# Kernel optimization log

Measured on AMD Instinct MI355X. Metric: run time of the kernel, lower is better.

The kernel has to match this reference:

```python
import jax, jax.numpy as jnp
import numpy as np

B, L, R = 4, 2048, 1024        # batch, seq_len, residual_dim
HID, EXP, K = 64, 2, 3          # hidden_dim, expansion_factor, conv_kernel_size
D = HID * EXP                   # ssm_input_dim = 128
N = HID                         # SSM state size = 64


def setup_inputs() -> dict:
    key = jax.random.key(0)
    ks = jax.random.split(key, 16)
    g = lambda k, s: jax.random.normal(k, s, dtype=jnp.float32) * 0.02
    inp = {
        "up_x":   jax.random.normal(ks[0], (B, L, R), dtype=jnp.float32),
        "W_up":   g(ks[1], (R, 2 * D)),
        "b_up":   g(ks[2], (2 * D,)),
        "conv_w": g(ks[3], (D, K)),          # depthwise Conv1d weight [C,1,K] squeezed
        "conv_b": g(ks[4], (D,)),
        "W_delta": g(ks[5], (D, D)),
        "b_delta": g(ks[6], (D,)),
        "W_B":    g(ks[7], (D, N)),
        "b_B":    g(ks[8], (N,)),
        "W_C":    g(ks[9], (D, N)),
        "b_C":    g(ks[10], (N,)),
        "A_log":  jnp.log(jnp.broadcast_to(jnp.arange(1, N + 1, dtype=jnp.float32), (D, N))),
        "D_skip": jnp.ones((D,), dtype=jnp.float32),
        "W_down": g(ks[11], (D, R)),
        "b_down": g(ks[12], (R,)),
    }
    return inp


def reference(up_x, W_up, b_up, conv_w, conv_b, W_delta, b_delta,
              W_B, b_B, W_C, b_C, A_log, D_skip, W_down, b_down):
    Lq = up_x.shape[1]
    u = up_x @ W_up + b_up                               # [B,L,2D]
    left, right = jnp.split(u, 2, axis=-1)               # each [B,L,D]

    # causal depthwise conv (pad left K-1, truncate to L)
    xp = jnp.pad(left, ((0, 0), (K - 1, 0), (0, 0)))     # [B,L+K-1,D]
    conv = sum(conv_w[:, k] * xp[:, k:k + Lq, :] for k in range(K)) + conv_b
    x = jax.nn.silu(conv)                                # [B,L,D]

    # S6 selective scan
    delta = jax.nn.softplus(x @ W_delta + b_delta)       # [B,L,D]
    Bm = x @ W_B + b_B                                   # [B,L,N]
    Cm = x @ W_C + b_C                                   # [B,L,N]
    A = -jnp.exp(A_log)                                  # [D,N]
    dA = jnp.exp(delta[..., None] * A)                   # [B,L,D,N]
    dBx = delta[..., None] * Bm[:, :, None, :] * x[..., None]  # [B,L,D,N]

    def step(h, inputs):
        dA_t, dBx_t, C_t = inputs                        # [B,D,N],[B,D,N],[B,N]
        h = dA_t * h + dBx_t
        y_t = jnp.einsum('bdn,bn->bd', h, C_t)
        return h, y_t

    h0 = jnp.zeros((up_x.shape[0], D, N), dtype=x.dtype)
    _, ys = jax.lax.scan(step, h0, (jnp.swapaxes(dA, 0, 1),
                                    jnp.swapaxes(dBx, 0, 1),
                                    jnp.swapaxes(Cm, 0, 1)))
    y = jnp.swapaxes(ys, 0, 1) + D_skip * x              # [B,L,D]

    gated = y * jax.nn.silu(right)                       # SiLU gate
    return gated @ W_down + b_down                       # [B,L,R]
```

## Files before the change

### kernel.cpp

```cpp
#include <hip/hip_runtime.h>
#include <math.h>

#define B_ 4
#define L_ 2048
#define R_ 1024
#define D_ 128
#define N_ 64
#define TWO_D 256
#define M_ (B_*L_)

#define LSTR 68

typedef __attribute__((ext_vector_type(8))) short bf16x8;
typedef __attribute__((ext_vector_type(4))) float f32x4;

__device__ __forceinline__ float silu_f(float z) {
    return z / (1.0f + __expf(-z));
}

__device__ __forceinline__ float softplus_f(float z) {
    return fmaxf(z, 0.0f) + log1pf(__expf(-fabsf(z)));
}

__device__ __forceinline__ short f2bf(float f) {
    union { float f; unsigned int u; } v; v.f = f;
    unsigned int r = v.u + 0x7FFF + ((v.u >> 16) & 1);
    return (short)(r >> 16);
}

__global__ __launch_bounds__(256) void gemm_up_mfma(
    const float* __restrict__ A,
    const float* __restrict__ W,
    const float* __restrict__ bias,
    float* __restrict__ C)
{
    __shared__ short Al[64 * LSTR];
    __shared__ short Bl[64 * LSTR];

    int lid = blockIdx.x;
    int xcd = lid & 7;
    int slot = lid >> 3;
    int bm = xcd * 16 + (slot >> 2);
    int bn = slot & 3;

    int tid = threadIdx.x;
    int w = tid >> 6, l = tid & 63;
    int lm = l & 15, q = l >> 4;
    int wm = (w & 1) * 32, wn = (w >> 1) * 32;

    f32x4 acc00 = {0,0,0,0}, acc01 = {0,0,0,0}, acc10 = {0,0,0,0}, acc11 = {0,0,0,0};

    int ar = tid >> 2, ak = (tid & 3) * 8;
    int bcol = tid & 63, bk = (tid >> 6) * 8;

    const float* Ag = A + (size_t)(bm * 64 + ar) * 1024 + ak;
    const float* Wg = W + (size_t)bn * 64 + bcol;

    for (int kt = 0; kt < 1024; kt += 32) {
        float4 a0 = *(const float4*)(Ag + kt);
        float4 a1 = *(const float4*)(Ag + kt + 4);
        bf16x8 ap;
        ap[0] = f2bf(a0.x); ap[1] = f2bf(a0.y); ap[2] = f2bf(a0.z); ap[3] = f2bf(a0.w);
        ap[4] = f2bf(a1.x); ap[5] = f2bf(a1.y); ap[6] = f2bf(a1.z); ap[7] = f2bf(a1.w);
        *(bf16x8*)&Al[ar * LSTR + ak] = ap;

        bf16x8 bp;
        #pragma unroll
        for (int j = 0; j < 8; j++)
            bp[j] = f2bf(Wg[(size_t)(kt + bk + j) * TWO_D]);
        *(bf16x8*)&Bl[bcol * LSTR + bk] = bp;

        __syncthreads();

        bf16x8 af0 = *(bf16x8*)&Al[(wm + lm) * LSTR + q * 8];
        bf16x8 af1 = *(bf16x8*)&Al[(wm + 16 + lm) * LSTR + q * 8];
        bf16x8 bf0 = *(bf16x8*)&Bl[(wn + lm) * LSTR + q * 8];
        bf16x8 bf1 = *(bf16x8*)&Bl[(wn + 16 + lm) * LSTR + q * 8];

        acc00 = __builtin_amdgcn_mfma_f32_16x16x32_bf16(af0, bf0, acc00, 0, 0, 0);
        acc01 = __builtin_amdgcn_mfma_f32_16x16x32_bf16(af0, bf1, acc01, 0, 0, 0);
        acc10 = __builtin_amdgcn_mfma_f32_16x16x32_bf16(af1, bf0, acc10, 0, 0, 0);
        acc11 = __builtin_amdgcn_mfma_f32_16x16x32_bf16(af1, bf1, acc11, 0, 0, 0);

        __syncthreads();
    }

    #pragma unroll
    for (int i = 0; i < 4; i++) {
        int r0 = bm * 64 + wm + q * 4 + i;
        int r1 = r0 + 16;
        int c0 = bn * 64 + wn + lm;
        int c1 = c0 + 16;
        C[(size_t)r0 * TWO_D + c0] = acc00[i] + bias[c0];
        C[(size_t)r0 * TWO_D + c1] = acc01[i] + bias[c1];
        C[(size_t)r1 * TWO_D + c0] = acc10[i] + bias[c0];
        C[(size_t)r1 * TWO_D + c1] = acc11[i] + bias[c1];
    }
}

__global__ __launch_bounds__(256) void conv_silu_kernel(
    const float* __restrict__ u,
    const float* __restrict__ conv_w,
    const float* __restrict__ conv_b,
    float* __restrict__ x)
{
    int idx = blockIdx.x * 256 + threadIdx.x;
    if (idx >= M_ * D_) return;
    int r = idx >> 7;
    int c = idx & 127;
    int t = r & (L_ - 1);

    float w0 = conv_w[c * 3 + 0];
    float w1 = conv_w[c * 3 + 1];
    float w2 = conv_w[c * 3 + 2];

    float v2 = u[(size_t)r * TWO_D + c];
    float v1 = (t >= 1) ? u[(size_t)(r - 1) * TWO_D + c] : 0.0f;
    float v0 = (t >= 2) ? u[(size_t)(r - 2) * TWO_D + c] : 0.0f;

    float z = fmaf(w0, v0, fmaf(w1, v1, fmaf(w2, v2, conv_b[c])));
    x[idx] = silu_f(z);
}

__global__ __launch_bounds__(256) void proj_mfma(
    const float* __restrict__ x,
    const float* __restrict__ W_delta, const float* __restrict__ b_delta,
    const float* __restrict__ W_B,     const float* __restrict__ b_B,
    const float* __restrict__ W_C,     const float* __restrict__ b_C,
    float* __restrict__ delta,
    float* __restrict__ Bm,
    float* __restrict__ Cm)
{
    __shared__ short Al[64 * LSTR];
    __shared__ short Bl[64 * LSTR];

    int lid = blockIdx.x;
    int xcd = lid & 7;
    int slot = lid >> 3;
    int bm = xcd * 16 + (slot >> 2);
    int bn = slot & 3;

    const float* Wsel; const float* bsel; int wstride;
    if (bn < 2)       { Wsel = W_delta + bn * 64; bsel = b_delta + bn * 64; wstride = 128; }
    else if (bn == 2) { Wsel = W_B;               bsel = b_B;               wstride = 64;  }
    else              { Wsel = W_C;               bsel = b_C;               wstride = 64;  }

    int tid = threadIdx.x;
    int w = tid >> 6, l = tid & 63;
    int lm = l & 15, q = l >> 4;
    int wm = (w & 1) * 32, wn = (w >> 1) * 32;

    f32x4 acc00 = {0,0,0,0}, acc01 = {0,0,0,0}, acc10 = {0,0,0,0}, acc11 = {0,0,0,0};

    int ar = tid >> 2, ak = (tid & 3) * 8;
    int bcol = tid & 63, bk = (tid >> 6) * 8;

    const float* Ag = x + (size_t)(bm * 64 + ar) * D_ + ak;
    const float* Wg = Wsel + bcol;

    for (int kt = 0; kt < 128; kt += 32) {
        float4 a0 = *(const float4*)(Ag + kt);
        float4 a1 = *(const float4*)(Ag + kt + 4);
        bf16x8 ap;
        ap[0] = f2bf(a0.x); ap[1] = f2bf(a0.y); ap[2] = f2bf(a0.z); ap[3] = f2bf(a0.w);
        ap[4] = f2bf(a1.x); ap[5] = f2bf(a1.y); ap[6] = f2bf(a1.z); ap[7] = f2bf(a1.w);
        *(bf16x8*)&Al[ar * LSTR + ak] = ap;

        bf16x8 bp;
        #pragma unroll
        for (int j = 0; j < 8; j++)
            bp[j] = f2bf(Wg[(size_t)(kt + bk + j) * wstride]);
        *(bf16x8*)&Bl[bcol * LSTR + bk] = bp;

        __syncthreads();

        bf16x8 af0 = *(bf16x8*)&Al[(wm + lm) * LSTR + q * 8];
        bf16x8 af1 = *(bf16x8*)&Al[(wm + 16 + lm) * LSTR + q * 8];
        bf16x8 bf0 = *(bf16x8*)&Bl[(wn + lm) * LSTR + q * 8];
        bf16x8 bf1 = *(bf16x8*)&Bl[(wn + 16 + lm) * LSTR + q * 8];

        acc00 = __builtin_amdgcn_mfma_f32_16x16x32_bf16(af0, bf0, acc00, 0, 0, 0);
        acc01 = __builtin_amdgcn_mfma_f32_16x16x32_bf16(af0, bf1, acc01, 0, 0, 0);
        acc10 = __builtin_amdgcn_mfma_f32_16x16x32_bf16(af1, bf0, acc10, 0, 0, 0);
        acc11 = __builtin_amdgcn_mfma_f32_16x16x32_bf16(af1, bf1, acc11, 0, 0, 0);

        __syncthreads();
    }

    #pragma unroll
    for (int i = 0; i < 4; i++) {
        int r0 = bm * 64 + wm + q * 4 + i;
        int r1 = r0 + 16;
        int c0 = wn + lm;
        int c1 = c0 + 16;
        float v00 = acc00[i] + bsel[c0];
        float v01 = acc01[i] + bsel[c1];
        float v10 = acc10[i] + bsel[c0];
        float v11 = acc11[i] + bsel[c1];
        if (bn < 2) {
            int cc0 = bn * 64 + c0, cc1 = bn * 64 + c1;
            delta[(size_t)r0 * D_ + cc0] = softplus_f(v00);
            delta[(size_t)r0 * D_ + cc1] = softplus_f(v01);
            delta[(size_t)r1 * D_ + cc0] = softplus_f(v10);
            delta[(size_t)r1 * D_ + cc1] = softplus_f(v11);
        } else if (bn == 2) {
            Bm[(size_t)r0 * N_ + c0] = v00;
            Bm[(size_t)r0 * N_ + c1] = v01;
            Bm[(size_t)r1 * N_ + c0] = v10;
            Bm[(size_t)r1 * N_ + c1] = v11;
        } else {
            Cm[(size_t)r0 * N_ + c0] = v00;
            Cm[(size_t)r0 * N_ + c1] = v01;
            Cm[(size_t)r1 * N_ + c0] = v10;
            Cm[(size_t)r1 * N_ + c1] = v11;
        }
    }
}

template<int LOG_NC>
__global__ __launch_bounds__(256) void scan_sumA(
    const float* __restrict__ delta,
    const float* __restrict__ x,
    const float* __restrict__ Bm,
    const float* __restrict__ A_log,
    float* __restrict__ ch_aprod,
    float* __restrict__ ch_h)
{
    constexpr int NCt = 1 << LOG_NC;
    constexpr int TCt = L_ >> LOG_NC;

    int wid = blockIdx.x * 4 + (threadIdx.x >> 6);
    int l = threadIdx.x & 63;
    int g = l >> 4, j = l & 15;
    int c = wid & (NCt - 1);
    int dq = (wid >> LOG_NC) & 31;
    int b = wid >> (LOG_NC + 5);
    int d = dq * 4 + g;

    const float LOG2E = 1.44269504089f;
    float4 Ar = *(const float4*)&A_log[d * N_ + j * 4];
    float Ai0 = -__expf(Ar.x) * LOG2E;
    float Ai1 = -__expf(Ar.y) * LOG2E;
    float Ai2 = -__expf(Ar.z) * LOG2E;
    float Ai3 = -__expf(Ar.w) * LOG2E;

    size_t row0 = (size_t)b * L_ + c * TCt;
    const float* dp = delta + row0 * D_ + d;
    const float* xp = x     + row0 * D_ + d;
    const float* bp = Bm    + row0 * N_ + j * 4;

    float h0 = 0, h1 = 0, h2 = 0, h3 = 0;
    float S = 0;

    #pragma unroll 8
    for (int t = 0; t < TCt; t++) {
        float dl = dp[t * D_];
        float xv = xp[t * D_];
        float4 bv = *(const float4*)&bp[t * N_];
        float e0 = exp2f(dl * Ai0);
        float e1 = exp2f(dl * Ai1);
        float e2 = exp2f(dl * Ai2);
        float e3 = exp2f(dl * Ai3);
        float dbx = dl * xv;
        h0 = fmaf(e0, h0, dbx * bv.x);
        h1 = fmaf(e1, h1, dbx * bv.y);
        h2 = fmaf(e2, h2, dbx * bv.z);
        h3 = fmaf(e3, h3, dbx * bv.w);
        S += dl;
    }

    size_t ci = (((size_t)b * D_ + d) * NCt + c) * N_ + j * 4;
    *(float4*)&ch_aprod[ci] = make_float4(exp2f(Ai0 * S), exp2f(Ai1 * S),
                                          exp2f(Ai2 * S), exp2f(Ai3 * S));
    *(float4*)&ch_h[ci]     = make_float4(h0, h1, h2, h3);
}

template<int LOG_NC>
__global__ __launch_bounds__(256) void scan_prefix(
    float* __restrict__ aprod_hin,
    const float* __restrict__ ch_h)
{
    constexpr int NCt = 1 << LOG_NC;
    int idx = blockIdx.x * 256 + threadIdx.x;
    int n = idx & 63;
    int rest = idx >> 6;
    size_t base = (size_t)rest * NCt * N_ + n;
    float h = 0.0f;
    #pragma unroll 8
    for (int c = 0; c < NCt; c++) {
        size_t o = base + (size_t)c * N_;
        float a  = aprod_hin[o];
        float hh = ch_h[o];
        aprod_hin[o] = h;
        h = fmaf(a, h, hh);
    }
}

template<int LOG_NC>
__global__ __launch_bounds__(256) void scan_outB(
    const float* __restrict__ delta,
    const float* __restrict__ x,
    const float* __restrict__ Bm,
    const float* __restrict__ Cm,
    const float* __restrict__ A_log,
    const float* __restrict__ D_skip,
    const float* __restrict__ hin,
    float* __restrict__ y)
{
    constexpr int NCt = 1 << LOG_NC;
    constexpr int TCt = L_ >> LOG_NC;

    int wid = blockIdx.x * 4 + (threadIdx.x >> 6);
    int l = threadIdx.x & 63;
    int g = l >> 4, j = l & 15;
    int c = wid & (NCt - 1);
    int dq = (wid >> LOG_NC) & 31;
    int b = wid >> (LOG_NC + 5);
    int d = dq * 4 + g;

    const float LOG2E = 1.44269504089f;
    float4 Ar = *(const float4*)&A_log[d * N_ + j * 4];
    float Ai0 = -__expf(Ar.x) * LOG2E;
    float Ai1 = -__expf(Ar.y) * LOG2E;
    float Ai2 = -__expf(Ar.z) * LOG2E;
    float Ai3 = -__expf(Ar.w) * LOG2E;
    float dsk = D_skip[d];

    float4 hv = *(const float4*)&hin[(((size_t)b * D_ + d) * NCt + c) * N_ + j * 4];
    float h0 = hv.x, h1 = hv.y, h2 = hv.z, h3 = hv.w;

    size_t row0 = (size_t)b * L_ + c * TCt;
    const float* dp = delta + row0 * D_ + d;
    const float* xp = x     + row0 * D_ + d;
    const float* bp = Bm    + row0 * N_ + j * 4;
    const float* cp = Cm    + row0 * N_ + j * 4;
    float*       yp = y     + row0 * D_ + d;

    #pragma unroll 8
    for (int t = 0; t < TCt; t++) {
        float dl = dp[t * D_];
        float xv = xp[t * D_];
        float4 bv = *(const float4*)&bp[t * N_];
        float4 cv = *(const float4*)&cp[t * N_];
        float e0 = exp2f(dl * Ai0);
        float e1 = exp2f(dl * Ai1);
        float e2 = exp2f(dl * Ai2);
        float e3 = exp2f(dl * Ai3);
        float dbx = dl * xv;
        h0 = fmaf(e0, h0, dbx * bv.x);
        h1 = fmaf(e1, h1, dbx * bv.y);
        h2 = fmaf(e2, h2, dbx * bv.z);
        h3 = fmaf(e3, h3, dbx * bv.w);
        float p = fmaf(h0, cv.x, fmaf(h1, cv.y, fmaf(h2, cv.z, h3 * cv.w)));
        p += __shfl_xor(p, 1, 64);
        p += __shfl_xor(p, 2, 64);
        p += __shfl_xor(p, 4, 64);
        p += __shfl_xor(p, 8, 64);
        if (j == 0) yp[t * D_] = fmaf(dsk, xv, p);
    }
}

__global__ __launch_bounds__(256) void gemm_down_mfma(
    const float* __restrict__ y,
    const float* __restrict__ u,
    const float* __restrict__ W,
    const float* __restrict__ bias,
    float* __restrict__ out)
{
    __shared__ short Al[64 * LSTR];
    __shared__ short Bl[64 * LSTR];

    int lid = blockIdx.x;
    int xcd = lid & 7;
    int slot = lid >> 3;
    int bm = xcd * 16 + (slot >> 4);
    int bn = slot & 15;

    int tid = threadIdx.x;
    int w = tid >> 6, l = tid & 63;
    int lm = l & 15, q = l >> 4;
    int wm = (w & 1) * 32, wn = (w >> 1) * 32;

    f32x4 acc00 = {0,0,0,0}, acc01 = {0,0,0,0}, acc10 = {0,0,0,0}, acc11 = {0,0,0,0};

    int ar = tid >> 2, ak = (tid & 3) * 8;
    int bcol = tid & 63, bk = (tid >> 6) * 8;

    const float* Yg = y + (size_t)(bm * 64 + ar) * D_ + ak;
    const float* Ug = u + (size_t)(bm * 64 + ar) * TWO_D + D_ + ak;
    const float* Wg = W + (size_t)bn * 64 + bcol;

    for (int kt = 0; kt < 128; kt += 32) {
        float4 y0 = *(const float4*)(Yg + kt);
        float4 y1 = *(const float4*)(Yg + kt + 4);
        float4 g0 = *(const float4*)(Ug + kt);
        float4 g1 = *(const float4*)(Ug + kt + 4);
        bf16x8 ap;
        ap[0] = f2bf(y0.x * silu_f(g0.x)); ap[1] = f2bf(y0.y * silu_f(g0.y));
        ap[2] = f2bf(y0.z * silu_f(g0.z)); ap[3] = f2bf(y0.w * silu_f(g0.w));
        ap[4] = f2bf(y1.x * silu_f(g1.x)); ap[5] = f2bf(y1.y * silu_f(g1.y));
        ap[6] = f2bf(y1.z * silu_f(g1.z)); ap[7] = f2bf(y1.w * silu_f(g1.w));
        *(bf16x8*)&Al[ar * LSTR + ak] = ap;

        bf16x8 bp;
        #pragma unroll
        for (int j = 0; j < 8; j++)
            bp[j] = f2bf(Wg[(size_t)(kt + bk + j) * R_]);
        *(bf16x8*)&Bl[bcol * LSTR + bk] = bp;

        __syncthreads();

        bf16x8 af0 = *(bf16x8*)&Al[(wm + lm) * LSTR + q * 8];
        bf16x8 af1 = *(bf16x8*)&Al[(wm + 16 + lm) * LSTR + q * 8];
        bf16x8 bf0 = *(bf16x8*)&Bl[(wn + lm) * LSTR + q * 8];
        bf16x8 bf1 = *(bf16x8*)&Bl[(wn + 16 + lm) * LSTR + q * 8];

        acc00 = __builtin_amdgcn_mfma_f32_16x16x32_bf16(af0, bf0, acc00, 0, 0, 0);
        acc01 = __builtin_amdgcn_mfma_f32_16x16x32_bf16(af0, bf1, acc01, 0, 0, 0);
        acc10 = __builtin_amdgcn_mfma_f32_16x16x32_bf16(af1, bf0, acc10, 0, 0, 0);
        acc11 = __builtin_amdgcn_mfma_f32_16x16x32_bf16(af1, bf1, acc11, 0, 0, 0);

        __syncthreads();
    }

    #pragma unroll
    for (int i = 0; i < 4; i++) {
        int r0 = bm * 64 + wm + q * 4 + i;
        int r1 = r0 + 16;
        int c0 = bn * 64 + wn + lm;
        int c1 = c0 + 16;
        out[(size_t)r0 * R_ + c0] = acc00[i] + bias[c0];
        out[(size_t)r0 * R_ + c1] = acc01[i] + bias[c1];
        out[(size_t)r1 * R_ + c0] = acc10[i] + bias[c0];
        out[(size_t)r1 * R_ + c1] = acc11[i] + bias[c1];
    }
}

extern "C" void kernel_launch(void* const* d_in, const int* in_sizes, int n_in,
                              void* d_out, int out_size, void* d_ws, size_t ws_size,
                              hipStream_t stream)
{
    const float* up_x    = (const float*)d_in[0];
    const float* W_up    = (const float*)d_in[1];
    const float* b_up    = (const float*)d_in[2];
    const float* conv_w  = (const float*)d_in[3];
    const float* conv_b  = (const float*)d_in[4];
    const float* W_delta = (const float*)d_in[5];
    const float* b_delta = (const float*)d_in[6];
    const float* W_B     = (const float*)d_in[7];
    const float* b_B     = (const float*)d_in[8];
    const float* W_C     = (const float*)d_in[9];
    const float* b_C     = (const float*)d_in[10];
    const float* A_log   = (const float*)d_in[11];
    const float* D_skip  = (const float*)d_in[12];
    const float* W_down  = (const float*)d_in[13];
    const float* b_down  = (const float*)d_in[14];

    float* out = (float*)d_out;
    float* ws  = (float*)d_ws;

    float* u     = ws;
    float* x     = u + (size_t)M_ * TWO_D;
    float* delta = x + (size_t)M_ * D_;
    float* Bm    = delta + (size_t)M_ * D_;
    float* Cm    = Bm + (size_t)M_ * N_;
    float* y     = Cm + (size_t)M_ * N_;
    float* ch_aprod = y + (size_t)M_ * D_;
    bool big = ws_size >= (size_t)41943040;

    gemm_up_mfma<<<(TWO_D / 64) * (M_ / 64), 256, 0, stream>>>(
        up_x, W_up, b_up, u);

    conv_silu_kernel<<<(M_ * D_ + 255) / 256, 256, 0, stream>>>(
        u, conv_w, conv_b, x);

    proj_mfma<<<4 * (M_ / 64), 256, 0, stream>>>(
        x, W_delta, b_delta, W_B, b_B, W_C, b_C, delta, Bm, Cm);

    if (big) {
        constexpr int LNC = 6;
        float* ch_h = ch_aprod + (size_t)B_ * D_ * (1 << LNC) * N_;
        scan_sumA<LNC><<<(B_ * (D_ / 4) * (1 << LNC)) / 4, 256, 0, stream>>>(
            delta, x, Bm, A_log, ch_aprod, ch_h);
        scan_prefix<LNC><<<(B_ * D_ * N_) / 256, 256, 0, stream>>>(
            ch_aprod, ch_h);
        scan_outB<LNC><<<(B_ * (D_ / 4) * (1 << LNC)) / 4, 256, 0, stream>>>(
            delta, x, Bm, Cm, A_log, D_skip, ch_aprod, y);
    } else {
        constexpr int LNC = 5;
        float* ch_h = ch_aprod + (size_t)B_ * D_ * (1 << LNC) * N_;
        scan_sumA<LNC><<<(B_ * (D_ / 4) * (1 << LNC)) / 4, 256, 0, stream>>>(
            delta, x, Bm, A_log, ch_aprod, ch_h);
        scan_prefix<LNC><<<(B_ * D_ * N_) / 256, 256, 0, stream>>>(
            ch_aprod, ch_h);
        scan_outB<LNC><<<(B_ * (D_ / 4) * (1 << LNC)) / 4, 256, 0, stream>>>(
            delta, x, Bm, Cm, A_log, D_skip, ch_aprod, y);
    }

    gemm_down_mfma<<<16 * (M_ / 64), 256, 0, stream>>>(
        y, u, W_down, b_down, out);
}
```

Measured before the change: 223.9 us.

## Split-K the up-projection GEMM and fuse partial reduction into conv kernel

The up-projection GEMM now splits K=1024 into two halves across twice as many blocks. Each half writes unbiased partials into reused workspace buffers (the delta and y regions). A new conv_gate kernel sums the two partials, adds the bias, writes the right (gate) half of u and computes the causal conv plus SiLU for the left half. This aims to raise occupancy for a GEMM that had few blocks per CU, at the cost of extra global traffic for the partials and for re-reading neighbouring rows. The byte packing is also moved into a shared pack8 helper.

```diff
diff --git a/kernel.cpp b/kernel.cpp
--- a/kernel.cpp
+++ b/kernel.cpp
@@ -28,11 +28,18 @@
     return (short)(r >> 16);
 }
 
-__global__ __launch_bounds__(256) void gemm_up_mfma(
+__device__ __forceinline__ bf16x8 pack8(float4 a, float4 b) {
+    bf16x8 r;
+    r[0] = f2bf(a.x); r[1] = f2bf(a.y); r[2] = f2bf(a.z); r[3] = f2bf(a.w);
+    r[4] = f2bf(b.x); r[5] = f2bf(b.y); r[6] = f2bf(b.z); r[7] = f2bf(b.w);
+    return r;
+}
+
+__global__ __launch_bounds__(256) void gemm_up_splitk(
     const float* __restrict__ A,
     const float* __restrict__ W,
-    const float* __restrict__ bias,
-    float* __restrict__ C)
+    float* __restrict__ P0,
+    float* __restrict__ P1)
 {
     __shared__ short Al[64 * LSTR];
     __shared__ short Bl[64 * LSTR];
@@ -40,8 +47,12 @@
     int lid = blockIdx.x;
     int xcd = lid & 7;
     int slot = lid >> 3;
-    int bm = xcd * 16 + (slot >> 2);
-    int bn = slot & 3;
+    int bm = xcd * 16 + (slot >> 3);
+    int r3 = slot & 7;
+    int bn = r3 & 3;
+    int split = r3 >> 2;
+    float* P = split ? P1 : P0;
+    int k0 = split * 512;
 
     int tid = threadIdx.x;
     int w = tid >> 6, l = tid & 63;
@@ -53,22 +64,24 @@
     int ar = tid >> 2, ak = (tid & 3) * 8;
     int bcol = tid & 63, bk = (tid >> 6) * 8;
 
-    const float* Ag = A + (size_t)(bm * 64 + ar) * 1024 + ak;
-    const float* Wg = W + (size_t)bn * 64 + bcol;
-
-    for (int kt = 0; kt < 1024; kt += 32) {
+    const float* Ag = A + (size_t)(bm * 64 + ar) * 1024 + k0 + ak;
+    const float* Wg = W + (size_t)(k0) * TWO_D + (size_t)bn * 64 + bcol;
+
+    for (int kt = 0; kt < 512; kt += 32) {
         float4 a0 = *(const float4*)(Ag + kt);
         float4 a1 = *(const float4*)(Ag + kt + 4);
-        bf16x8 ap;
-        ap[0] = f2bf(a0.x); ap[1] = f2bf(a0.y); ap[2] = f2bf(a0.z); ap[3] = f2bf(a0.w);
-        ap[4] = f2bf(a1.x); ap[5] = f2bf(a1.y); ap[6] = f2bf(a1.z); ap[7] = f2bf(a1.w);
-        *(bf16x8*)&Al[ar * LSTR + ak] = ap;
-
-        bf16x8 bp;
-        #pragma unroll
-        for (int j = 0; j < 8; j++)
-            bp[j] = f2bf(Wg[(size_t)(kt + bk + j) * TWO_D]);
-        *(bf16x8*)&Bl[bcol * LSTR + bk] = bp;
+        *(bf16x8*)&Al[ar * LSTR + ak] = pack8(a0, a1);
+
+        float w0 = Wg[(size_t)(kt + bk + 0) * TWO_D];
+        float w1 = Wg[(size_t)(kt + bk + 1) * TWO_D];
+        float w2 = Wg[(size_t)(kt + bk + 2) * TWO_D];
+        float w3 = Wg[(size_t)(kt + bk + 3) * TWO_D];
+        float w4 = Wg[(size_t)(kt + bk + 4) * TWO_D];
+        float w5 = Wg[(size_t)(kt + bk + 5) * TWO_D];
+        float w6 = Wg[(size_t)(kt + bk + 6) * TWO_D];
+        float w7 = Wg[(size_t)(kt + bk + 7) * TWO_D];
+        *(bf16x8*)&Bl[bcol * LSTR + bk] =
+            pack8(make_float4(w0, w1, w2, w3), make_float4(w4, w5, w6, w7));
 
         __syncthreads();
 
@@ -91,35 +104,40 @@
         int r1 = r0 + 16;
         int c0 = bn * 64 + wn + lm;
         int c1 = c0 + 16;
-        C[(size_t)r0 * TWO_D + c0] = acc00[i] + bias[c0];
-        C[(size_t)r0 * TWO_D + c1] = acc01[i] + bias[c1];
-        C[(size_t)r1 * TWO_D + c0] = acc10[i] + bias[c0];
-        C[(size_t)r1 * TWO_D + c1] = acc11[i] + bias[c1];
-    }
-}
-
-__global__ __launch_bounds__(256) void conv_silu_kernel(
-    const float* __restrict__ u,
+        P[(size_t)r0 * TWO_D + c0] = acc00[i];
+        P[(size_t)r0 * TWO_D + c1] = acc01[i];
+        P[(size_t)r1 * TWO_D + c0] = acc10[i];
+        P[(size_t)r1 * TWO_D + c1] = acc11[i];
+    }
+}
+
+__global__ __launch_bounds__(256) void conv_gate_kernel(
+    const float* __restrict__ P0,
+    const float* __restrict__ P1,
+    const float* __restrict__ b_up,
     const float* __restrict__ conv_w,
     const float* __restrict__ conv_b,
-    float* __restrict__ x)
+    float* __restrict__ x,
+    float* __restrict__ u)
 {
     int idx = blockIdx.x * 256 + threadIdx.x;
-    if (idx >= M_ * D_) return;
-    int r = idx >> 7;
-    int c = idx & 127;
+    int r = idx >> 8;
+    int c = idx & 255;
+    float bb = b_up[c];
+    float p = P0[idx] + P1[idx] + bb;
+
+    if (c >= 128) {
+        u[idx] = p;
+        return;
+    }
     int t = r & (L_ - 1);
-
     float w0 = conv_w[c * 3 + 0];
     float w1 = conv_w[c * 3 + 1];
     float w2 = conv_w[c * 3 + 2];
-
-    float v2 = u[(size_t)r * TWO_D + c];
-    float v1 = (t >= 1) ? u[(size_t)(r - 1) * TWO_D + c] : 0.0f;
-    float v0 = (t >= 2) ? u[(size_t)(r - 2) * TWO_D + c] : 0.0f;
-
-    float z = fmaf(w0, v0, fmaf(w1, v1, fmaf(w2, v2, conv_b[c])));
-    x[idx] = silu_f(z);
+    float v1 = (t >= 1) ? P0[idx - 256] + P1[idx - 256] + bb : 0.0f;
+    float v0 = (t >= 2) ? P0[idx - 512] + P1[idx - 512] + bb : 0.0f;
+    float z = fmaf(w0, v0, fmaf(w1, v1, fmaf(w2, p, conv_b[c])));
+    x[(size_t)r * D_ + c] = silu_f(z);
 }
 
 __global__ __launch_bounds__(256) void proj_mfma(
@@ -161,16 +179,18 @@
     for (int kt = 0; kt < 128; kt += 32) {
         float4 a0 = *(const float4*)(Ag + kt);
         float4 a1 = *(const float4*)(Ag + kt + 4);
-        bf16x8 ap;
-        ap[0] = f2bf(a0.x); ap[1] = f2bf(a0.y); ap[2] = f2bf(a0.z); ap[3] = f2bf(a0.w);
-        ap[4] = f2bf(a1.x); ap[5] = f2bf(a1.y); ap[6] = f2bf(a1.z); ap[7] = f2bf(a1.w);
-        *(bf16x8*)&Al[ar * LSTR + ak] = ap;
-
-        bf16x8 bp;
-        #pragma unroll
-        for (int j = 0; j < 8; j++)
-            bp[j] = f2bf(Wg[(size_t)(kt + bk + j) * wstride]);
-        *(bf16x8*)&Bl[bcol * LSTR + bk] = bp;
+        *(bf16x8*)&Al[ar * LSTR + ak] = pack8(a0, a1);
+
+        float w0 = Wg[(size_t)(kt + bk + 0) * wstride];
+        float w1 = Wg[(size_t)(kt + bk + 1) * wstride];
+        float w2 = Wg[(size_t)(kt + bk + 2) * wstride];
+        float w3 = Wg[(size_t)(kt + bk + 3) * wstride];
+        float w4 = Wg[(size_t)(kt + bk + 4) * wstride];
+        float w5 = Wg[(size_t)(kt + bk + 5) * wstride];
+        float w6 = Wg[(size_t)(kt + bk + 6) * wstride];
+        float w7 = Wg[(size_t)(kt + bk + 7) * wstride];
+        *(bf16x8*)&Bl[bcol * LSTR + bk] =
+            pack8(make_float4(w0, w1, w2, w3), make_float4(w4, w5, w6, w7));
 
         __syncthreads();
 
@@ -395,18 +415,22 @@
         float4 y1 = *(const float4*)(Yg + kt + 4);
         float4 g0 = *(const float4*)(Ug + kt);
         float4 g1 = *(const float4*)(Ug + kt + 4);
-        bf16x8 ap;
-        ap[0] = f2bf(y0.x * silu_f(g0.x)); ap[1] = f2bf(y0.y * silu_f(g0.y));
-        ap[2] = f2bf(y0.z * silu_f(g0.z)); ap[3] = f2bf(y0.w * silu_f(g0.w));
-        ap[4] = f2bf(y1.x * silu_f(g1.x)); ap[5] = f2bf(y1.y * silu_f(g1.y));
-        ap[6] = f2bf(y1.z * silu_f(g1.z)); ap[7] = f2bf(y1.w * silu_f(g1.w));
-        *(bf16x8*)&Al[ar * LSTR + ak] = ap;
-
-        bf16x8 bp;
-        #pragma unroll
-        for (int j = 0; j < 8; j++)
-            bp[j] = f2bf(Wg[(size_t)(kt + bk + j) * R_]);
-        *(bf16x8*)&Bl[bcol * LSTR + bk] = bp;
+        float4 a0 = make_float4(y0.x * silu_f(g0.x), y0.y * silu_f(g0.y),
+                                y0.z * silu_f(g0.z), y0.w * silu_f(g0.w));
+        float4 a1 = make_float4(y1.x * silu_f(g1.x), y1.y * silu_f(g1.y),
+                                y1.z * silu_f(g1.z), y1.w * silu_f(g1.w));
+        *(bf16x8*)&Al[ar * LSTR + ak] = pack8(a0, a1);
+
+        float w0 = Wg[(size_t)(kt + bk + 0) * R_];
+        float w1 = Wg[(size_t)(kt + bk + 1) * R_];
+        float w2 = Wg[(size_t)(kt + bk + 2) * R_];
+        float w3 = Wg[(size_t)(kt + bk + 3) * R_];
+        float w4 = Wg[(size_t)(kt + bk + 4) * R_];
+        float w5 = Wg[(size_t)(kt + bk + 5) * R_];
+        float w6 = Wg[(size_t)(kt + bk + 6) * R_];
+        float w7 = Wg[(size_t)(kt + bk + 7) * R_];
+        *(bf16x8*)&Bl[bcol * LSTR + bk] =
+            pack8(make_float4(w0, w1, w2, w3), make_float4(w4, w5, w6, w7));
 
         __syncthreads();
 
@@ -468,11 +492,13 @@
     float* ch_aprod = y + (size_t)M_ * D_;
     bool big = ws_size >= (size_t)41943040;
 
-    gemm_up_mfma<<<(TWO_D / 64) * (M_ / 64), 256, 0, stream>>>(
-        up_x, W_up, b_up, u);
-
-    conv_silu_kernel<<<(M_ * D_ + 255) / 256, 256, 0, stream>>>(
-        u, conv_w, conv_b, x);
+    float* P0 = delta;
+    float* P1 = y;
+
+    gemm_up_splitk<<<1024, 256, 0, stream>>>(up_x, W_up, P0, P1);
+
+    conv_gate_kernel<<<(M_ * TWO_D) / 256, 256, 0, stream>>>(
+        P0, P1, b_up, conv_w, conv_b, x, u);
 
     proj_mfma<<<4 * (M_ / 64), 256, 0, stream>>>(
         x, W_delta, b_delta, W_B, b_B, W_C, b_C, delta, Bm, Cm);
```

New measurement: 218.7 us. 1.02x faster.
